# Optimization experiments

Measured on AMD Instinct MI355X. Metric: run time of the kernel, lower is better.

## Reference

```python
import jax, jax.numpy as jnp
import numpy as np

N_SRC, N_DST, E = 10000, 10000, 640000
S, T, O, H = 128, 128, 128, 4
D = O // H


def setup_inputs() -> dict:
    key = jax.random.key(0)
    ks = jax.random.split(key, 12)
    f = lambda k, shape, fan: jax.random.normal(k, shape, dtype=jnp.float32) / np.float32(np.sqrt(fan))
    return {
        "x_src": jax.random.normal(ks[0], (N_SRC, S), dtype=jnp.float32),
        "x_dst": jax.random.normal(ks[1], (N_DST, T), dtype=jnp.float32),
        "W_pred1": f(ks[2], (S, T), T),
        "b_pred1": jnp.zeros((S,), jnp.float32),
        "W_pred2": f(ks[3], (S, S), S),
        "b_pred2": jnp.zeros((S,), jnp.float32),
        "W_res": f(ks[4], (H * D, S), S),
        "W_src": f(ks[5], (H * D, S), S),
        "W_dst": f(ks[6], (H * D, T), T),
        "att_src": jax.random.normal(ks[7], (1, H, D), dtype=jnp.float32) * 0.01,
        "att_dst": jax.random.normal(ks[8], (1, H, D), dtype=jnp.float32) * 0.01,
        "W_self": f(ks[9], (H * D, T), T),
        "b_self": jnp.zeros((H * D,), jnp.float32),
        "edge_src": jax.random.randint(ks[10], (E,), 0, N_SRC),
        "edge_dst": jax.random.randint(ks[11], (E,), 0, N_DST),
        "num_dst": N_DST,
    }


def reference(x_src, x_dst, W_pred1, b_pred1, W_pred2, b_pred2, W_res, W_src, W_dst,
              att_src, att_dst, W_self, b_self, edge_src, edge_dst, num_dst):
    h, d = att_src.shape[1], att_src.shape[2]
    # residual prediction path: pred_mlp(x_dst) = Lin2(ReLU(Lin1(x_dst)))
    pred = jax.nn.relu(x_dst @ W_pred1.T + b_pred1) @ W_pred2.T + b_pred2  # [Ndst,S]
    residual = x_src[edge_src] - pred[edge_dst]                            # [E,S]
    # per-node attention logits (equivalent to gather-then-dot, cheaper)
    a_s = ((x_src @ W_src.T).reshape(-1, h, d) * att_src).sum(-1)          # [Nsrc,H]
    a_d = ((x_dst @ W_dst.T).reshape(-1, h, d) * att_dst).sum(-1)          # [Ndst,H]
    alpha = jax.nn.leaky_relu(a_s[edge_src] + a_d[edge_dst], 0.2)          # [E,H]
    # edge softmax over incoming edges of each destination node
    amax = jax.ops.segment_max(alpha, edge_dst, num_segments=num_dst)      # [Ndst,H]
    ex = jnp.exp(alpha - amax[edge_dst])
    denom = jax.ops.segment_sum(ex, edge_dst, num_segments=num_dst)
    alpha = ex / (denom[edge_dst] + 1e-16)                                 # [E,H]
    # attention-weighted aggregation of transformed residuals
    msg = (residual @ W_res.T).reshape(-1, h, d) * alpha[:, :, None]       # [E,H,D]
    agg = jax.ops.segment_sum(msg.reshape(-1, h * d), edge_dst, num_segments=num_dst)
    return agg + x_dst @ W_self.T + b_self                                 # [Ndst,H*D]
```

## Files before the change

### kernel.cpp

```cpp
#include <hip/hip_runtime.h>
#include <hip/hip_bf16.h>

#define LEAKY 0.2f
#define CAP 160
#define CAPB 8192
#define CHUNK 2048
#define GSTRIDE 32

#define FMA4(A, S, V) do { (A).x += (S)*(V).x; (A).y += (S)*(V).y; (A).z += (S)*(V).z; (A).w += (S)*(V).w; } while (0)

typedef __attribute__((ext_vector_type(8))) short bf16x8;
typedef __attribute__((ext_vector_type(4))) float f32x4;

struct GemmJob {
  const float* X; const float* W; const float* B; float* Y;
  int M; int relu; int bf16out;
  const float* vvec;
  float* aout;
};

__device__ __forceinline__ unsigned short f2bf(float f) {
  unsigned int u = __float_as_uint(f);
  u += 0x7FFFu + ((u >> 16) & 1u);
  return (unsigned short)(u >> 16);
}
__device__ __forceinline__ float bf2f(unsigned short h) {
  return __uint_as_float(((unsigned int)h) << 16);
}

__device__ __forceinline__ bf16x8 pack8(const float4& a, const float4& b) {
  bf16x8 r;
  r[0] = (short)__builtin_bit_cast(unsigned short, __float2bfloat16(a.x));
  r[1] = (short)__builtin_bit_cast(unsigned short, __float2bfloat16(a.y));
  r[2] = (short)__builtin_bit_cast(unsigned short, __float2bfloat16(a.z));
  r[3] = (short)__builtin_bit_cast(unsigned short, __float2bfloat16(a.w));
  r[4] = (short)__builtin_bit_cast(unsigned short, __float2bfloat16(b.x));
  r[5] = (short)__builtin_bit_cast(unsigned short, __float2bfloat16(b.y));
  r[6] = (short)__builtin_bit_cast(unsigned short, __float2bfloat16(b.z));
  r[7] = (short)__builtin_bit_cast(unsigned short, __float2bfloat16(b.w));
  return r;
}

__device__ __forceinline__ void gemm128_mfma(
    const float* __restrict__ X, const float* __restrict__ W,
    const float* __restrict__ B, float* __restrict__ Y,
    int M, int relu, int bf16out, int row0,
    const float* __restrict__ vvec, float* __restrict__ aout) {
  if (row0 >= M) return;
  const int tid = threadIdx.x;
  const int wv = tid >> 6;
  const int ln = tid & 63;
  const int lr = ln & 15;
  const int kg = ln >> 4;

  const f32x4 zero = {0.f, 0.f, 0.f, 0.f};
  f32x4 acc[2][8];
#pragma unroll
  for (int mt = 0; mt < 2; mt++)
#pragma unroll
    for (int nt = 0; nt < 8; nt++) acc[mt][nt] = zero;

  float4 av0 = make_float4(0.f, 0.f, 0.f, 0.f), av1 = av0;

  const int r0 = row0 + wv * 32 + lr;
  const int r1 = r0 + 16;
  const int rc0 = r0 < M ? r0 : M - 1;
  const int rc1 = r1 < M ? r1 : M - 1;
  const float* xp0 = X + (size_t)rc0 * 128 + kg * 8;
  const float* xp1 = X + (size_t)rc1 * 128 + kg * 8;
  const float* wp  = W + (size_t)lr * 128 + kg * 8;

#pragma unroll
  for (int k0 = 0; k0 < 128; k0 += 32) {
    float4 xa0 = *(const float4*)(xp0 + k0);
    float4 xb0 = *(const float4*)(xp0 + k0 + 4);
    float4 xa1 = *(const float4*)(xp1 + k0);
    float4 xb1 = *(const float4*)(xp1 + k0 + 4);
    bf16x8 a0 = pack8(xa0, xb0);
    bf16x8 a1 = pack8(xa1, xb1);
#pragma unroll
    for (int nt = 0; nt < 8; nt++) {
      const float* wq = wp + (size_t)nt * 16 * 128 + k0;
      bf16x8 bw = pack8(*(const float4*)wq, *(const float4*)(wq + 4));
      acc[0][nt] = __builtin_amdgcn_mfma_f32_16x16x32_bf16(a0, bw, acc[0][nt], 0, 0, 0);
      acc[1][nt] = __builtin_amdgcn_mfma_f32_16x16x32_bf16(a1, bw, acc[1][nt], 0, 0, 0);
    }
    if (vvec) {
      const float4* vv = (const float4*)vvec + (k0 + kg * 8);
#pragma unroll
      for (int j = 0; j < 4; j++) {
        float4 v4 = vv[j];
        float s0 = (j == 0) ? xa0.x : (j == 1) ? xa0.y : (j == 2) ? xa0.z : xa0.w;
        float s1 = (j == 0) ? xa1.x : (j == 1) ? xa1.y : (j == 2) ? xa1.z : xa1.w;
        FMA4(av0, s0, v4); FMA4(av1, s1, v4);
      }
#pragma unroll
      for (int j = 0; j < 4; j++) {
        float4 v4 = vv[4 + j];
        float s0 = (j == 0) ? xb0.x : (j == 1) ? xb0.y : (j == 2) ? xb0.z : xb0.w;
        float s1 = (j == 0) ? xb1.x : (j == 1) ? xb1.y : (j == 2) ? xb1.z : xb1.w;
        FMA4(av0, s0, v4); FMA4(av1, s1, v4);
      }
    }
  }

  if (vvec) {
    av0.x += __shfl_xor(av0.x, 16, 64); av0.y += __shfl_xor(av0.y, 16, 64);
    av0.z += __shfl_xor(av0.z, 16, 64); av0.w += __shfl_xor(av0.w, 16, 64);
    av0.x += __shfl_xor(av0.x, 32, 64); av0.y += __shfl_xor(av0.y, 32, 64);
    av0.z += __shfl_xor(av0.z, 32, 64); av0.w += __shfl_xor(av0.w, 32, 64);
    av1.x += __shfl_xor(av1.x, 16, 64); av1.y += __shfl_xor(av1.y, 16, 64);
    av1.z += __shfl_xor(av1.z, 16, 64); av1.w += __shfl_xor(av1.w, 16, 64);
    av1.x += __shfl_xor(av1.x, 32, 64); av1.y += __shfl_xor(av1.y, 32, 64);
    av1.z += __shfl_xor(av1.z, 32, 64); av1.w += __shfl_xor(av1.w, 32, 64);
    if (kg == 0) {
      if (r0 < M) *(float4*)(aout + (size_t)r0 * 4) = av0;
      if (r1 < M) *(float4*)(aout + (size_t)r1 * 4) = av1;
    }
  }

  float bv[8];
#pragma unroll
  for (int nt = 0; nt < 8; nt++) bv[nt] = B ? B[nt * 16 + lr] : 0.f;

  const int rbase = row0 + wv * 32 + kg * 4;
#pragma unroll
  for (int mt = 0; mt < 2; mt++) {
#pragma unroll
    for (int i = 0; i < 4; i++) {
      int r = rbase + mt * 16 + i;
      if (r >= M) continue;
      if (bf16out) {
        unsigned short* yb = (unsigned short*)Y + (size_t)r * 128 + lr;
#pragma unroll
        for (int nt = 0; nt < 8; nt++) {
          float o = acc[mt][nt][i] + bv[nt];
          if (relu) o = fmaxf(o, 0.f);
          yb[nt * 16] = f2bf(o);
        }
      } else {
        float* yp = Y + (size_t)r * 128 + lr;
#pragma unroll
        for (int nt = 0; nt < 8; nt++) {
          float o = acc[mt][nt][i] + bv[nt];
          if (relu) o = fmaxf(o, 0.f);
          yp[nt * 16] = o;
        }
      }
    }
  }
}

__global__ __launch_bounds__(256) void phase1(
    const float* __restrict__ Wsrc, const float* __restrict__ attsrc,
    const float* __restrict__ Wdst, const float* __restrict__ attdst,
    const float* __restrict__ W_res, const float* __restrict__ W2,
    const float* __restrict__ b2,
    GemmJob jA,
    float* __restrict__ v_src, float* __restrict__ v_dst,
    float* __restrict__ Wc, float* __restrict__ bc,
    const int* __restrict__ edge_src, const int* __restrict__ edge_dst,
    int* __restrict__ gcnt, int* __restrict__ bin,
    int E, int Nd, int NB, int GA, int Q1, int T1) {
  __shared__ int bsm[CHUNK + 3 * CAP];
  int bx = blockIdx.x, tid = threadIdx.x;
  int u = (bx & 7) * Q1 + (bx >> 3);
  if (u >= T1) return;
  if (u == 0) {
    int which = tid >> 7, k = tid & 127;
    const float* W = which ? Wdst : Wsrc;
    const float* att = which ? attdst : attsrc;
    float* v = which ? v_dst : v_src;
    float s[4] = {0.f, 0.f, 0.f, 0.f};
#pragma unroll
    for (int h = 0; h < 4; h++)
      for (int d = 0; d < 32; d++)
        s[h] += W[(size_t)(h * 32 + d) * 128 + k] * att[h * 32 + d];
#pragma unroll
    for (int h = 0; h < 4; h++) v[k * 4 + h] = s[h];
  } else if (u == 1) {
    if (tid < 128) {
      float s = 0.f;
      for (int i = 0; i < 128; i++) s += W_res[(size_t)tid * 128 + i] * b2[i];
      bc[tid] = s;
    }
  } else if (u < 66) {
    int id = (u - 2) * 256 + tid;
    int o = id >> 7, j = id & 127;
    float s = 0.f;
    for (int i = 0; i < 128; i++) s += W_res[(size_t)o * 128 + i] * W2[(size_t)i * 128 + j];
    Wc[(size_t)o * 128 + j] = s;
  } else if (u < 66 + GA) {
    gemm128_mfma(jA.X, jA.W, jA.B, jA.Y, jA.M, jA.relu, jA.bf16out,
                 (u - 66) * 128, jA.vvec, jA.aout);
  } else {
    int* pk    = bsm;
    int* hist  = bsm + CHUNK;
    int* gbase = hist + CAP;
    int* lcur  = gbase + CAP;
    int e0 = (u - 66 - GA) * CHUNK;
    int n = E - e0; if (n > CHUNK) n = CHUNK;
    if (n <= 0) return;
    for (int i = tid; i < NB; i += 256) hist[i] = 0;
    __syncthreads();
    for (int i = tid; i < n; i += 256) {
      int s = edge_src[e0 + i], d = edge_dst[e0 + i];
      pk[i] = (s << 14) | d;
      atomicAdd(&hist[d >> 6], 1);
    }
    __syncthreads();
    for (int b = tid; b < NB; b += 256) {
      gbase[b] = hist[b] ? atomicAdd(&gcnt[b * GSTRIDE], hist[b]) : 0;
      lcur[b] = 0;
    }
    __syncthreads();
    for (int i = tid; i < n; i += 256) {
      int p = pk[i];
      int b = (p & 16383) >> 6;
      int off = gbase[b] + atomicAdd(&lcur[b], 1);
      if (off < CAPB) bin[(size_t)b * CAPB + off] = p;
    }
  }
}

__global__ __launch_bounds__(256) void phase2(
    GemmJob j0, GemmJob j1, GemmJob j2,
    const int* __restrict__ gcnt, const int* __restrict__ bin,
    int* __restrict__ sorted_src, int* __restrict__ rstart, int* __restrict__ rend,
    int Nd, int G, int Q2, int T2) {
  __shared__ int ssm[128];
  int bx = blockIdx.x, tid = threadIdx.x;
  int u = (bx % 6) * Q2 + bx / 6;
  if (u >= T2) return;
  if (u < 3 * G) {
    GemmJob J = (u < G) ? j0 : (u < 2 * G) ? j1 : j2;
    gemm128_mfma(J.X, J.W, J.B, J.Y, J.M, J.relu, J.bf16out, (u % G) * 128, J.vvec, J.aout);
  } else {
    int b = u - 3 * G;
    int* hist2 = ssm;
    int* lcur2 = ssm + 64;
    int cnt = gcnt[b * GSTRIDE]; if (cnt > CAPB) cnt = CAPB;
    size_t base = (size_t)b * CAPB;
    if (tid < 64) hist2[tid] = 0;
    __syncthreads();
    for (int i = tid; i < cnt; i += 256) atomicAdd(&hist2[bin[base + i] & 63], 1);
    __syncthreads();
    if (tid < 64) {
      int v = hist2[tid];
      int incl = v;
#pragma unroll
      for (int off = 1; off < 64; off <<= 1) {
        int t = __shfl_up(incl, off, 64);
        if (tid >= off) incl += t;
      }
      int st = incl - v;
      lcur2[tid] = st;
      int dst = (b << 6) + tid;
      if (dst < Nd) {
        rstart[dst] = (int)base + st;
        rend[dst]   = (int)base + st + v;
      }
    }
    __syncthreads();
    for (int i = tid; i < cnt; i += 256) {
      int p = bin[base + i];
      int j = p & 63;
      int lp = atomicAdd(&lcur2[j], 1);
      sorted_src[base + lp] = p >> 14;
    }
  }
}

__global__ __launch_bounds__(256) void phase3(
    const int* __restrict__ rstart, const int* __restrict__ rend,
    const int* __restrict__ sorted_src,
    const float* __restrict__ a_s, const float* __restrict__ a_d,
    const unsigned short* __restrict__ u_src, const float* __restrict__ u_pred,
    const float* __restrict__ self_o, float* __restrict__ out, int Nd) {
  __shared__ float smem[1920];
  int bx = blockIdx.x, tid = threadIdx.x;
  int half = tid >> 7;
  int t = tid & 127;
  int dst = bx * 2 + half;
  if (dst >= Nd) return;

  float* wbuf  = smem + half * 640;
  int* srcbuf  = (int*)(smem + 1280) + half * 160;
  float4* red4 = (float4*)(smem + 1600);
  float4* redv = (float4*)(smem + 1616) + half * 32;
  float* inv_s = smem + 1872 + half * 4;
  float* sA_s  = smem + 1880 + half * 4;

  int start = rstart[dst];
  int deg = rend[dst] - start;
  float4 ad4 = *(const float4*)(a_d + (size_t)dst * 4);
  float s0 = 0.f, s1 = 0.f, s2 = 0.f, s3 = 0.f;
  for (int i = t; i < deg; i += 128) {
    int src = sorted_src[start + i];
    float4 as4 = *(const float4*)(a_s + (size_t)src * 4);
    float l0 = as4.x + ad4.x; l0 = l0 > 0.f ? l0 : LEAKY * l0;
    float l1 = as4.y + ad4.y; l1 = l1 > 0.f ? l1 : LEAKY * l1;
    float l2 = as4.z + ad4.z; l2 = l2 > 0.f ? l2 : LEAKY * l2;
    float l3 = as4.w + ad4.w; l3 = l3 > 0.f ? l3 : LEAKY * l3;
    float w0 = __expf(l0), w1 = __expf(l1), w2 = __expf(l2), w3 = __expf(l3);
    if (i < CAP) {
      wbuf[i * 4 + 0] = w0; wbuf[i * 4 + 1] = w1;
      wbuf[i * 4 + 2] = w2; wbuf[i * 4 + 3] = w3;
      srcbuf[i] = src;
    }
    s0 += w0; s1 += w1; s2 += w2; s3 += w3;
  }
  int wave = tid >> 6;
#pragma unroll
  for (int off = 32; off > 0; off >>= 1) {
    s0 += __shfl_xor(s0, off, 64);
    s1 += __shfl_xor(s1, off, 64);
    s2 += __shfl_xor(s2, off, 64);
    s3 += __shfl_xor(s3, off, 64);
  }
  if ((tid & 63) == 0) red4[wave] = make_float4(s0, s1, s2, s3);
  __syncthreads();
  if (t == 0) {
    float4 A = red4[half * 2], B = red4[half * 2 + 1];
    float dx = A.x + B.x, dy = A.y + B.y, dz = A.z + B.z, dw = A.w + B.w;
    inv_s[0] = 1.f / (dx + 1e-16f); sA_s[0] = dx * inv_s[0];
    inv_s[1] = 1.f / (dy + 1e-16f); sA_s[1] = dy * inv_s[1];
    inv_s[2] = 1.f / (dz + 1e-16f); sA_s[2] = dz * inv_s[2];
    inv_s[3] = 1.f / (dw + 1e-16f); sA_s[3] = dw * inv_s[3];
  }
  __syncthreads();

  int c4 = t & 31, rgrp = t >> 5, h = c4 >> 3;
  int coff = c4 * 4;
  float4 acc0 = make_float4(0.f,0.f,0.f,0.f), acc1 = acc0, acc2 = acc0, acc3 = acc0;
  int cap = deg < CAP ? deg : CAP;
  int i = rgrp;
  for (; i + 12 < cap; i += 16) {
    int sA = srcbuf[i], sB = srcbuf[i + 4], sC = srcbuf[i + 8], sD = srcbuf[i + 12];
    float wA = wbuf[i * 4 + h], wB = wbuf[(i + 4) * 4 + h];
    float wC = wbuf[(i + 8) * 4 + h], wD = wbuf[(i + 12) * 4 + h];
    ushort4 hA = *(const ushort4*)(u_src + (size_t)sA * 128 + coff);
    ushort4 hB = *(const ushort4*)(u_src + (size_t)sB * 128 + coff);
    ushort4 hC = *(const ushort4*)(u_src + (size_t)sC * 128 + coff);
    ushort4 hD = *(const ushort4*)(u_src + (size_t)sD * 128 + coff);
    float4 uA = make_float4(bf2f(hA.x), bf2f(hA.y), bf2f(hA.z), bf2f(hA.w));
    float4 uB = make_float4(bf2f(hB.x), bf2f(hB.y), bf2f(hB.z), bf2f(hB.w));
    float4 uC = make_float4(bf2f(hC.x), bf2f(hC.y), bf2f(hC.z), bf2f(hC.w));
    float4 uD = make_float4(bf2f(hD.x), bf2f(hD.y), bf2f(hD.z), bf2f(hD.w));
    FMA4(acc0, wA, uA); FMA4(acc1, wB, uB); FMA4(acc2, wC, uC); FMA4(acc3, wD, uD);
  }
  for (; i < cap; i += 4) {
    int s_ = srcbuf[i];
    float w = wbuf[i * 4 + h];
    ushort4 hh = *(const ushort4*)(u_src + (size_t)s_ * 128 + coff);
    float4 uu = make_float4(bf2f(hh.x), bf2f(hh.y), bf2f(hh.z), bf2f(hh.w));
    FMA4(acc0, w, uu);
  }
  if (deg > CAP) {
    float adh = (h == 0) ? ad4.x : (h == 1) ? ad4.y : (h == 2) ? ad4.z : ad4.w;
    for (int k = CAP + rgrp; k < deg; k += 4) {
      int src = sorted_src[start + k];
      float l = a_s[(size_t)src * 4 + h] + adh;
      l = l > 0.f ? l : LEAKY * l;
      float w = __expf(l);
      ushort4 hh = *(const ushort4*)(u_src + (size_t)src * 128 + coff);
      float4 uu = make_float4(bf2f(hh.x), bf2f(hh.y), bf2f(hh.z), bf2f(hh.w));
      FMA4(acc0, w, uu);
    }
  }
  float4 acc;
  acc.x = acc0.x + acc1.x + acc2.x + acc3.x;
  acc.y = acc0.y + acc1.y + acc2.y + acc3.y;
  acc.z = acc0.z + acc1.z + acc2.z + acc3.z;
  acc.w = acc0.w + acc1.w + acc2.w + acc3.w;
  acc.x += __shfl_xor(acc.x, 32, 64);
  acc.y += __shfl_xor(acc.y, 32, 64);
  acc.z += __shfl_xor(acc.z, 32, 64);
  acc.w += __shfl_xor(acc.w, 32, 64);
  if (t >= 64 && t < 96) redv[c4] = acc;
  __syncthreads();
  if (t < 32) {
    float4 r = redv[c4];
    acc.x += r.x; acc.y += r.y; acc.z += r.z; acc.w += r.w;
    float4 up = *(const float4*)(u_pred + (size_t)dst * 128 + coff);
    float4 so = *(const float4*)(self_o + (size_t)dst * 128 + coff);
    float iv = inv_s[h], sa = sA_s[h];
    float4 o;
    o.x = acc.x * iv - sa * up.x + so.x;
    o.y = acc.y * iv - sa * up.y + so.y;
    o.z = acc.z * iv - sa * up.z + so.z;
    o.w = acc.w * iv - sa * up.w + so.w;
    *(float4*)(out + (size_t)dst * 128 + coff) = o;
  }
}

extern "C" void kernel_launch(void* const* d_in, const int* in_sizes, int n_in,
                              void* d_out, int out_size, void* d_ws, size_t ws_size,
                              hipStream_t stream) {
  const float* x_src   = (const float*)d_in[0];
  const float* x_dst   = (const float*)d_in[1];
  const float* W_pred1 = (const float*)d_in[2];
  const float* b_pred1 = (const float*)d_in[3];
  const float* W_pred2 = (const float*)d_in[4];
  const float* b_pred2 = (const float*)d_in[5];
  const float* W_res   = (const float*)d_in[6];
  const float* W_src   = (const float*)d_in[7];
  const float* W_dst   = (const float*)d_in[8];
  const float* att_src = (const float*)d_in[9];
  const float* att_dst = (const float*)d_in[10];
  const float* W_self  = (const float*)d_in[11];
  const float* b_self  = (const float*)d_in[12];
  const int* edge_src  = (const int*)d_in[13];
  const int* edge_dst  = (const int*)d_in[14];
  int Ns = in_sizes[0] / 128;
  int Nd = in_sizes[1] / 128;
  int E  = in_sizes[13];
  float* out = (float*)d_out;
  int NB = (Nd + 63) >> 6;

  char* ws = (char*)d_ws;
  auto alloc = [&](size_t bytes) -> char* {
    char* p = ws;
    ws += (bytes + 255) & ~(size_t)255;
    return p;
  };
  float* relu1  = (float*)alloc((size_t)Nd * 128 * 4);
  unsigned short* u_src = (unsigned short*)alloc((size_t)Ns * 128 * 2);
  float* u_pred = (float*)alloc((size_t)Nd * 128 * 4);
  float* self_o = (float*)alloc((size_t)Nd * 128 * 4);
  float* a_s    = (float*)alloc((size_t)Ns * 4 * 4);
  float* a_d    = (float*)alloc((size_t)Nd * 4 * 4);
  float* v_src  = (float*)alloc(128 * 4 * 4);
  float* v_dst  = (float*)alloc(128 * 4 * 4);
  float* Wc     = (float*)alloc(128 * 128 * 4);
  float* bc     = (float*)alloc(128 * 4);
  int* gcnt     = (int*)alloc((size_t)NB * GSTRIDE * 4);
  int* rstart   = (int*)alloc((size_t)Nd * 4);
  int* rend     = (int*)alloc((size_t)Nd * 4);
  int* bin      = (int*)alloc((size_t)NB * CAPB * 4);
  int* sorted_src = (int*)alloc((size_t)NB * CAPB * 4);

  hipMemsetAsync(gcnt, 0, (size_t)NB * GSTRIDE * sizeof(int), stream);

  int GA  = (Nd + 127) / 128;
  int NCH = (E + CHUNK - 1) / CHUNK;
  int T1 = 66 + GA + NCH;
  int Q1 = (T1 + 7) / 8;
  GemmJob jA{ x_dst, W_pred1, b_pred1, relu1, Nd, 1, 0, nullptr, nullptr };
  hipLaunchKernelGGL(phase1, dim3(Q1 * 8), dim3(256), 0, stream,
                     W_src, att_src, W_dst, att_dst, W_res, W_pred2, b_pred2, jA,
                     v_src, v_dst, Wc, bc, edge_src, edge_dst, gcnt, bin,
                     E, Nd, NB, GA, Q1, T1);

  int maxM = Ns > Nd ? Ns : Nd;
  int G  = (maxM + 127) / 128;
  int T2 = 3 * G + NB;
  int Q2 = (T2 + 5) / 6;
  GemmJob jB{ x_src, W_res,  nullptr, (float*)u_src, Ns, 0, 1, v_src, a_s };
  GemmJob jC{ x_dst, W_self, b_self,  self_o, Nd, 0, 0, v_dst, a_d };
  GemmJob jU{ relu1, Wc,     bc,      u_pred, Nd, 0, 0, nullptr, nullptr };
  hipLaunchKernelGGL(phase2, dim3(Q2 * 6), dim3(256), 0, stream,
                     jB, jC, jU, gcnt, bin, sorted_src, rstart, rend,
                     Nd, G, Q2, T2);

  hipLaunchKernelGGL(phase3, dim3((Nd + 1) / 2), dim3(256), 0, stream,
                     rstart, rend, sorted_src, a_s, a_d, u_src, u_pred, self_o, out, Nd);
}
```

Baseline: 157.3 us.

## Fuse three phases into one persistent cooperative kernel with grid syncs

Replaces the three separate kernel launches with one persistent cooperative kernel of up to 512 blocks. Each block loops over work units and the three stages are separated by grid.sync, with a fallback to three launches of a staged kernel. It also recomputes the attention projection vectors inside each GEMM unit rather than in a separate unit, moves the x_src/x_dst GEMMs into the first stage, and doubles the edge-binning chunk size. The aim is to remove launch gaps and tail idle time between phases. The costs are grid-barrier overhead, a fixed grid-stride loop that may balance work worse, redundant per-tile projection work, and possible occupancy limits from launch_bounds(256,2).

New measurement: 383.9 us. +144.1%, slower.

```diff
diff --git a/kernel.cpp b/kernel.cpp
--- a/kernel.cpp
+++ b/kernel.cpp
@@ -1,11 +1,15 @@
 #include <hip/hip_runtime.h>
 #include <hip/hip_bf16.h>
+#include <hip/hip_cooperative_groups.h>
+
+namespace cg = cooperative_groups;
 
 #define LEAKY 0.2f
 #define CAP 160
 #define CAPB 8192
-#define CHUNK 2048
+#define CHUNK 4096
 #define GSTRIDE 32
+#define GRID 512
 
 #define FMA4(A, S, V) do { (A).x += (S)*(V).x; (A).y += (S)*(V).y; (A).z += (S)*(V).z; (A).w += (S)*(V).w; } while (0)
 
@@ -15,8 +19,21 @@
 struct GemmJob {
   const float* X; const float* W; const float* B; float* Y;
   int M; int relu; int bf16out;
-  const float* vvec;
+  const float* Wv;
+  const float* attv;
   float* aout;
+};
+
+struct Params {
+  GemmJob jA, jB, jC, jU;
+  const float* W_res; const float* W2; const float* b2;
+  float* Wc; float* bc;
+  const int* edge_src; const int* edge_dst;
+  int* gcnt; int* bin; int* sorted_src; int* rstart; int* rend;
+  const float* a_s; const float* a_d;
+  const unsigned short* u_src; const float* u_pred; const float* self_o;
+  float* out;
+  int E, Nd, NB, GA, G, NCH, U0, U1, U2;
 };
 
 __device__ __forceinline__ unsigned short f2bf(float f) {
@@ -45,7 +62,7 @@
     const float* __restrict__ X, const float* __restrict__ W,
     const float* __restrict__ B, float* __restrict__ Y,
     int M, int relu, int bf16out, int row0,
-    const float* __restrict__ vvec, float* __restrict__ aout) {
+    const float* vvec, float* __restrict__ aout) {
   if (row0 >= M) return;
   const int tid = threadIdx.x;
   const int wv = tid >> 6;
@@ -151,138 +168,97 @@
   }
 }
 
-__global__ __launch_bounds__(256) void phase1(
-    const float* __restrict__ Wsrc, const float* __restrict__ attsrc,
-    const float* __restrict__ Wdst, const float* __restrict__ attdst,
-    const float* __restrict__ W_res, const float* __restrict__ W2,
-    const float* __restrict__ b2,
-    GemmJob jA,
-    float* __restrict__ v_src, float* __restrict__ v_dst,
-    float* __restrict__ Wc, float* __restrict__ bc,
-    const int* __restrict__ edge_src, const int* __restrict__ edge_dst,
-    int* __restrict__ gcnt, int* __restrict__ bin,
-    int E, int Nd, int NB, int GA, int Q1, int T1) {
-  __shared__ int bsm[CHUNK + 3 * CAP];
-  int bx = blockIdx.x, tid = threadIdx.x;
-  int u = (bx & 7) * Q1 + (bx >> 3);
-  if (u >= T1) return;
-  if (u == 0) {
-    int which = tid >> 7, k = tid & 127;
-    const float* W = which ? Wdst : Wsrc;
-    const float* att = which ? attdst : attsrc;
-    float* v = which ? v_dst : v_src;
-    float s[4] = {0.f, 0.f, 0.f, 0.f};
-#pragma unroll
-    for (int h = 0; h < 4; h++)
-      for (int d = 0; d < 32; d++)
-        s[h] += W[(size_t)(h * 32 + d) * 128 + k] * att[h * 32 + d];
-#pragma unroll
-    for (int h = 0; h < 4; h++) v[k * 4 + h] = s[h];
-  } else if (u == 1) {
-    if (tid < 128) {
+__device__ __forceinline__ void gemm_unit(const GemmJob& J, int row0, char* smemraw) {
+  const float* vvec = nullptr;
+  if (J.Wv) {
+    float* vl = (float*)smemraw;
+    for (int idx = threadIdx.x; idx < 512; idx += 256) {
+      int k = idx >> 2, h = idx & 3;
+      const float* wp = J.Wv + (size_t)(h * 32) * 128 + k;
+      const float* ap = J.attv + h * 32;
       float s = 0.f;
-      for (int i = 0; i < 128; i++) s += W_res[(size_t)tid * 128 + i] * b2[i];
-      bc[tid] = s;
-    }
-  } else if (u < 66) {
-    int id = (u - 2) * 256 + tid;
-    int o = id >> 7, j = id & 127;
-    float s = 0.f;
-    for (int i = 0; i < 128; i++) s += W_res[(size_t)o * 128 + i] * W2[(size_t)i * 128 + j];
-    Wc[(size_t)o * 128 + j] = s;
-  } else if (u < 66 + GA) {
-    gemm128_mfma(jA.X, jA.W, jA.B, jA.Y, jA.M, jA.relu, jA.bf16out,
-                 (u - 66) * 128, jA.vvec, jA.aout);
-  } else {
-    int* pk    = bsm;
-    int* hist  = bsm + CHUNK;
-    int* gbase = hist + CAP;
-    int* lcur  = gbase + CAP;
-    int e0 = (u - 66 - GA) * CHUNK;
-    int n = E - e0; if (n > CHUNK) n = CHUNK;
-    if (n <= 0) return;
-    for (int i = tid; i < NB; i += 256) hist[i] = 0;
+#pragma unroll 8
+      for (int d = 0; d < 32; d++) s += wp[(size_t)d * 128] * ap[d];
+      vl[idx] = s;
+    }
     __syncthreads();
-    for (int i = tid; i < n; i += 256) {
-      int s = edge_src[e0 + i], d = edge_dst[e0 + i];
-      pk[i] = (s << 14) | d;
-      atomicAdd(&hist[d >> 6], 1);
-    }
-    __syncthreads();
-    for (int b = tid; b < NB; b += 256) {
-      gbase[b] = hist[b] ? atomicAdd(&gcnt[b * GSTRIDE], hist[b]) : 0;
-      lcur[b] = 0;
-    }
-    __syncthreads();
-    for (int i = tid; i < n; i += 256) {
-      int p = pk[i];
-      int b = (p & 16383) >> 6;
-      int off = gbase[b] + atomicAdd(&lcur[b], 1);
-      if (off < CAPB) bin[(size_t)b * CAPB + off] = p;
-    }
-  }
-}
-
-__global__ __launch_bounds__(256) void phase2(
-    GemmJob j0, GemmJob j1, GemmJob j2,
-    const int* __restrict__ gcnt, const int* __restrict__ bin,
-    int* __restrict__ sorted_src, int* __restrict__ rstart, int* __restrict__ rend,
-    int Nd, int G, int Q2, int T2) {
-  __shared__ int ssm[128];
-  int bx = blockIdx.x, tid = threadIdx.x;
-  int u = (bx % 6) * Q2 + bx / 6;
-  if (u >= T2) return;
-  if (u < 3 * G) {
-    GemmJob J = (u < G) ? j0 : (u < 2 * G) ? j1 : j2;
-    gemm128_mfma(J.X, J.W, J.B, J.Y, J.M, J.relu, J.bf16out, (u % G) * 128, J.vvec, J.aout);
-  } else {
-    int b = u - 3 * G;
-    int* hist2 = ssm;
-    int* lcur2 = ssm + 64;
-    int cnt = gcnt[b * GSTRIDE]; if (cnt > CAPB) cnt = CAPB;
-    size_t base = (size_t)b * CAPB;
-    if (tid < 64) hist2[tid] = 0;
-    __syncthreads();
-    for (int i = tid; i < cnt; i += 256) atomicAdd(&hist2[bin[base + i] & 63], 1);
-    __syncthreads();
-    if (tid < 64) {
-      int v = hist2[tid];
-      int incl = v;
-#pragma unroll
-      for (int off = 1; off < 64; off <<= 1) {
-        int t = __shfl_up(incl, off, 64);
-        if (tid >= off) incl += t;
-      }
-      int st = incl - v;
-      lcur2[tid] = st;
-      int dst = (b << 6) + tid;
-      if (dst < Nd) {
-        rstart[dst] = (int)base + st;
-        rend[dst]   = (int)base + st + v;
-      }
-    }
-    __syncthreads();
-    for (int i = tid; i < cnt; i += 256) {
-      int p = bin[base + i];
-      int j = p & 63;
-      int lp = atomicAdd(&lcur2[j], 1);
-      sorted_src[base + lp] = p >> 14;
-    }
-  }
-}
-
-__global__ __launch_bounds__(256) void phase3(
-    const int* __restrict__ rstart, const int* __restrict__ rend,
-    const int* __restrict__ sorted_src,
-    const float* __restrict__ a_s, const float* __restrict__ a_d,
-    const unsigned short* __restrict__ u_src, const float* __restrict__ u_pred,
-    const float* __restrict__ self_o, float* __restrict__ out, int Nd) {
-  __shared__ float smem[1920];
-  int bx = blockIdx.x, tid = threadIdx.x;
+    vvec = vl;
+  }
+  gemm128_mfma(J.X, J.W, J.B, J.Y, J.M, J.relu, J.bf16out, row0, vvec, J.aout);
+}
+
+__device__ __forceinline__ void bin_unit(const Params& P, int c, char* smemraw) {
+  int* pk    = (int*)smemraw;
+  int* hist  = pk + CHUNK;
+  int* gbase = hist + CAP;
+  int* lcur  = gbase + CAP;
+  const int tid = threadIdx.x;
+  int e0 = c * CHUNK;
+  int n = P.E - e0; if (n > CHUNK) n = CHUNK;
+  for (int i = tid; i < P.NB; i += 256) hist[i] = 0;
+  __syncthreads();
+  for (int i = tid; i < n; i += 256) {
+    int s = P.edge_src[e0 + i], d = P.edge_dst[e0 + i];
+    pk[i] = (s << 14) | d;
+    atomicAdd(&hist[d >> 6], 1);
+  }
+  __syncthreads();
+  for (int b = tid; b < P.NB; b += 256) {
+    gbase[b] = hist[b] ? atomicAdd(&P.gcnt[b * GSTRIDE], hist[b]) : 0;
+    lcur[b] = 0;
+  }
+  __syncthreads();
+  for (int i = tid; i < n; i += 256) {
+    int p = pk[i];
+    int b = (p & 16383) >> 6;
+    int off = gbase[b] + atomicAdd(&lcur[b], 1);
+    if (off < CAPB) P.bin[(size_t)b * CAPB + off] = p;
+  }
+}
+
+__device__ __forceinline__ void sort_unit(const Params& P, int b, char* smemraw) {
+  int* hist2 = (int*)smemraw;
+  int* lcur2 = hist2 + 64;
+  const int tid = threadIdx.x;
+  int cnt = P.gcnt[b * GSTRIDE]; if (cnt > CAPB) cnt = CAPB;
+  size_t base = (size_t)b * CAPB;
+  if (tid < 64) hist2[tid] = 0;
+  __syncthreads();
+  for (int i = tid; i < cnt; i += 256) atomicAdd(&hist2[P.bin[base + i] & 63], 1);
+  __syncthreads();
+  if (tid < 64) {
+    int v = hist2[tid];
+    int incl = v;
+#pragma unroll
+    for (int off = 1; off < 64; off <<= 1) {
+      int t = __shfl_up(incl, off, 64);
+      if (tid >= off) incl += t;
+    }
+    int st = incl - v;
+    lcur2[tid] = st;
+    int dst = (b << 6) + tid;
+    if (dst < P.Nd) {
+      P.rstart[dst] = (int)base + st;
+      P.rend[dst]   = (int)base + st + v;
+    }
+  }
+  __syncthreads();
+  for (int i = tid; i < cnt; i += 256) {
+    int p = P.bin[base + i];
+    int j = p & 63;
+    int lp = atomicAdd(&lcur2[j], 1);
+    P.sorted_src[base + lp] = p >> 14;
+  }
+}
+
+__device__ __forceinline__ void agg_unit(const Params& P, int unit, char* smemraw) {
+  float* smem = (float*)smemraw;
+  const int tid = threadIdx.x;
   int half = tid >> 7;
   int t = tid & 127;
-  int dst = bx * 2 + half;
-  if (dst >= Nd) return;
+  int dst = unit * 2 + half;
+  bool act = dst < P.Nd;
+  int dstc = act ? dst : P.Nd - 1;
 
   float* wbuf  = smem + half * 640;
   int* srcbuf  = (int*)(smem + 1280) + half * 160;
@@ -291,13 +267,13 @@
   float* inv_s = smem + 1872 + half * 4;
   float* sA_s  = smem + 1880 + half * 4;
 
-  int start = rstart[dst];
-  int deg = rend[dst] - start;
-  float4 ad4 = *(const float4*)(a_d + (size_t)dst * 4);
+  int start = P.rstart[dstc];
+  int deg = act ? (P.rend[dstc] - start) : 0;
+  float4 ad4 = *(const float4*)(P.a_d + (size_t)dstc * 4);
   float s0 = 0.f, s1 = 0.f, s2 = 0.f, s3 = 0.f;
   for (int i = t; i < deg; i += 128) {
-    int src = sorted_src[start + i];
-    float4 as4 = *(const float4*)(a_s + (size_t)src * 4);
+    int src = P.sorted_src[start + i];
+    float4 as4 = *(const float4*)(P.a_s + (size_t)src * 4);
     float l0 = as4.x + ad4.x; l0 = l0 > 0.f ? l0 : LEAKY * l0;
     float l1 = as4.y + ad4.y; l1 = l1 > 0.f ? l1 : LEAKY * l1;
     float l2 = as4.z + ad4.z; l2 = l2 > 0.f ? l2 : LEAKY * l2;
@@ -339,10 +315,10 @@
     int sA = srcbuf[i], sB = srcbuf[i + 4], sC = srcbuf[i + 8], sD = srcbuf[i + 12];
     float wA = wbuf[i * 4 + h], wB = wbuf[(i + 4) * 4 + h];
     float wC = wbuf[(i + 8) * 4 + h], wD = wbuf[(i + 12) * 4 + h];
-    ushort4 hA = *(const ushort4*)(u_src + (size_t)sA * 128 + coff);
-    ushort4 hB = *(const ushort4*)(u_src + (size_t)sB * 128 + coff);
-    ushort4 hC = *(const ushort4*)(u_src + (size_t)sC * 128 + coff);
-    ushort4 hD = *(const ushort4*)(u_src + (size_t)sD * 128 + coff);
+    ushort4 hA = *(const ushort4*)(P.u_src + (size_t)sA * 128 + coff);
+    ushort4 hB = *(const ushort4*)(P.u_src + (size_t)sB * 128 + coff);
+    ushort4 hC = *(const ushort4*)(P.u_src + (size_t)sC * 128 + coff);
+    ushort4 hD = *(const ushort4*)(P.u_src + (size_t)sD * 128 + coff);
     float4 uA = make_float4(bf2f(hA.x), bf2f(hA.y), bf2f(hA.z), bf2f(hA.w));
     float4 uB = make_float4(bf2f(hB.x), bf2f(hB.y), bf2f(hB.z), bf2f(hB.w));
     float4 uC = make_float4(bf2f(hC.x), bf2f(hC.y), bf2f(hC.z), bf2f(hC.w));
@@ -352,18 +328,18 @@
   for (; i < cap; i += 4) {
     int s_ = srcbuf[i];
     float w = wbuf[i * 4 + h];
-    ushort4 hh = *(const ushort4*)(u_src + (size_t)s_ * 128 + coff);
+    ushort4 hh = *(const ushort4*)(P.u_src + (size_t)s_ * 128 + coff);
     float4 uu = make_float4(bf2f(hh.x), bf2f(hh.y), bf2f(hh.z), bf2f(hh.w));
     FMA4(acc0, w, uu);
   }
   if (deg > CAP) {
     float adh = (h == 0) ? ad4.x : (h == 1) ? ad4.y : (h == 2) ? ad4.z : ad4.w;
     for (int k = CAP + rgrp; k < deg; k += 4) {
-      int src = sorted_src[start + k];
-      float l = a_s[(size_t)src * 4 + h] + adh;
+      int src = P.sorted_src[start + k];
+      float l = P.a_s[(size_t)src * 4 + h] + adh;
       l = l > 0.f ? l : LEAKY * l;
       float w = __expf(l);
-      ushort4 hh = *(const ushort4*)(u_src + (size_t)src * 128 + coff);
+      ushort4 hh = *(const ushort4*)(P.u_src + (size_t)src * 128 + coff);
       float4 uu = make_float4(bf2f(hh.x), bf2f(hh.y), bf2f(hh.z), bf2f(hh.w));
       FMA4(acc0, w, uu);
     }
@@ -379,19 +355,78 @@
   acc.w += __shfl_xor(acc.w, 32, 64);
   if (t >= 64 && t < 96) redv[c4] = acc;
   __syncthreads();
-  if (t < 32) {
+  if (t < 32 && act) {
     float4 r = redv[c4];
     acc.x += r.x; acc.y += r.y; acc.z += r.z; acc.w += r.w;
-    float4 up = *(const float4*)(u_pred + (size_t)dst * 128 + coff);
-    float4 so = *(const float4*)(self_o + (size_t)dst * 128 + coff);
+    float4 up = *(const float4*)(P.u_pred + (size_t)dst * 128 + coff);
+    float4 so = *(const float4*)(P.self_o + (size_t)dst * 128 + coff);
     float iv = inv_s[h], sa = sA_s[h];
     float4 o;
     o.x = acc.x * iv - sa * up.x + so.x;
     o.y = acc.y * iv - sa * up.y + so.y;
     o.z = acc.z * iv - sa * up.z + so.z;
     o.w = acc.w * iv - sa * up.w + so.w;
-    *(float4*)(out + (size_t)dst * 128 + coff) = o;
-  }
+    *(float4*)(P.out + (size_t)dst * 128 + coff) = o;
+  }
+}
+
+__device__ __forceinline__ void run_stage(const Params& P, int stage, char* smemraw,
+                                          int bid, int grd) {
+  const int tid = threadIdx.x;
+  if (stage == 0) {
+    for (int u = bid; u < P.U0; u += grd) {
+      __syncthreads();
+      if (u < 64) {
+        int id = u * 256 + tid;
+        int o = id >> 7, j = id & 127;
+        float s = 0.f;
+        for (int i = 0; i < 128; i++) s += P.W_res[(size_t)o * 128 + i] * P.W2[(size_t)i * 128 + j];
+        P.Wc[(size_t)o * 128 + j] = s;
+      } else if (u == 64) {
+        if (tid < 128) {
+          float s = 0.f;
+          for (int i = 0; i < 128; i++) s += P.W_res[(size_t)tid * 128 + i] * P.b2[i];
+          P.bc[tid] = s;
+        }
+      } else if (u < 65 + P.GA) {
+        gemm_unit(P.jA, (u - 65) * 128, smemraw);
+      } else if (u < 65 + P.GA + P.G) {
+        gemm_unit(P.jB, (u - 65 - P.GA) * 128, smemraw);
+      } else if (u < 65 + P.GA + 2 * P.G) {
+        gemm_unit(P.jC, (u - 65 - P.GA - P.G) * 128, smemraw);
+      } else {
+        bin_unit(P, u - (65 + P.GA + 2 * P.G), smemraw);
+      }
+    }
+  } else if (stage == 1) {
+    for (int u = bid; u < P.U1; u += grd) {
+      __syncthreads();
+      if (u < P.G) gemm_unit(P.jU, u * 128, smemraw);
+      else sort_unit(P, u - P.G, smemraw);
+    }
+  } else {
+    for (int u = bid; u < P.U2; u += grd) {
+      __syncthreads();
+      agg_unit(P, u, smemraw);
+    }
+  }
+}
+
+__global__ __launch_bounds__(256, 2) void kmain(Params P) {
+  __shared__ __align__(16) char smemraw[18816];
+  cg::grid_group grid = cg::this_grid();
+  run_stage(P, 0, smemraw, blockIdx.x, gridDim.x);
+  __threadfence();
+  grid.sync();
+  run_stage(P, 1, smemraw, blockIdx.x, gridDim.x);
+  __threadfence();
+  grid.sync();
+  run_stage(P, 2, smemraw, blockIdx.x, gridDim.x);
+}
+
+__global__ __launch_bounds__(256, 2) void kstage(Params P, int stage) {
+  __shared__ __align__(16) char smemraw[18816];
+  run_stage(P, stage, smemraw, blockIdx.x, gridDim.x);
 }
 
 extern "C" void kernel_launch(void* const* d_in, const int* in_sizes, int n_in,
@@ -430,8 +465,6 @@
   float* self_o = (float*)alloc((size_t)Nd * 128 * 4);
   float* a_s    = (float*)alloc((size_t)Ns * 4 * 4);
   float* a_d    = (float*)alloc((size_t)Nd * 4 * 4);
-  float* v_src  = (float*)alloc(128 * 4 * 4);
-  float* v_dst  = (float*)alloc(128 * 4 * 4);
   float* Wc     = (float*)alloc(128 * 128 * 4);
   float* bc     = (float*)alloc(128 * 4);
   int* gcnt     = (int*)alloc((size_t)NB * GSTRIDE * 4);
@@ -443,26 +476,53 @@
   hipMemsetAsync(gcnt, 0, (size_t)NB * GSTRIDE * sizeof(int), stream);
 
   int GA  = (Nd + 127) / 128;
+  int maxM = Ns > Nd ? Ns : Nd;
+  int G   = (maxM + 127) / 128;
   int NCH = (E + CHUNK - 1) / CHUNK;
-  int T1 = 66 + GA + NCH;
-  int Q1 = (T1 + 7) / 8;
-  GemmJob jA{ x_dst, W_pred1, b_pred1, relu1, Nd, 1, 0, nullptr, nullptr };
-  hipLaunchKernelGGL(phase1, dim3(Q1 * 8), dim3(256), 0, stream,
-                     W_src, att_src, W_dst, att_dst, W_res, W_pred2, b_pred2, jA,
-                     v_src, v_dst, Wc, bc, edge_src, edge_dst, gcnt, bin,
-                     E, Nd, NB, GA, Q1, T1);
-
-  int maxM = Ns > Nd ? Ns : Nd;
-  int G  = (maxM + 127) / 128;
-  int T2 = 3 * G + NB;
-  int Q2 = (T2 + 5) / 6;
-  GemmJob jB{ x_src, W_res,  nullptr, (float*)u_src, Ns, 0, 1, v_src, a_s };
-  GemmJob jC{ x_dst, W_self, b_self,  self_o, Nd, 0, 0, v_dst, a_d };
-  GemmJob jU{ relu1, Wc,     bc,      u_pred, Nd, 0, 0, nullptr, nullptr };
-  hipLaunchKernelGGL(phase2, dim3(Q2 * 6), dim3(256), 0, stream,
-                     jB, jC, jU, gcnt, bin, sorted_src, rstart, rend,
-                     Nd, G, Q2, T2);
-
-  hipLaunchKernelGGL(phase3, dim3((Nd + 1) / 2), dim3(256), 0, stream,
-                     rstart, rend, sorted_src, a_s, a_d, u_src, u_pred, self_o, out, Nd);
-}
+
+  Params P;
+  P.jA = GemmJob{ x_dst, W_pred1, b_pred1, relu1, Nd, 1, 0, nullptr, nullptr, nullptr };
+  P.jB = GemmJob{ x_src, W_res,  nullptr, (float*)u_src, Ns, 0, 1, W_src, att_src, a_s };
+  P.jC = GemmJob{ x_dst, W_self, b_self,  self_o, Nd, 0, 0, W_dst, att_dst, a_d };
+  P.jU = GemmJob{ relu1, Wc,     bc,      u_pred, Nd, 0, 0, nullptr, nullptr, nullptr };
+  P.W_res = W_res; P.W2 = W_pred2; P.b2 = b_pred2;
+  P.Wc = Wc; P.bc = bc;
+  P.edge_src = edge_src; P.edge_dst = edge_dst;
+  P.gcnt = gcnt; P.bin = bin; P.sorted_src = sorted_src;
+  P.rstart = rstart; P.rend = rend;
+  P.a_s = a_s; P.a_d = a_d;
+  P.u_src = u_src; P.u_pred = u_pred; P.self_o = self_o;
+  P.out = out;
+  P.E = E; P.Nd = Nd; P.NB = NB; P.GA = GA; P.G = G; P.NCH = NCH;
+  P.U0 = 65 + GA + 2 * G + NCH;
+  P.U1 = G + NB;
+  P.U2 = (Nd + 1) / 2;
+
+  static int coopGrid = -2;
+  if (coopGrid == -2) {
+    int occ = 0, numCU = 256;
+    hipDeviceProp_t prop;
+    if (hipGetDeviceProperties(&prop, 0) == hipSuccess && prop.multiProcessorCount > 0)
+      numCU = prop.multiProcessorCount;
+    if (hipOccupancyMaxActiveBlocksPerMultiprocessor(&occ, kmain, 256, 0) == hipSuccess && occ > 0) {
+      long cap = (long)occ * numCU;
+      coopGrid = cap > GRID ? GRID : (int)cap;
+    } else {
+      coopGrid = -1;
+    }
+  }
+
+  bool done = false;
+  if (coopGrid > 0) {
+    void* args[] = { (void*)&P };
+    hipError_t le = hipLaunchCooperativeKernel((const void*)kmain, dim3(coopGrid), dim3(256),
+                                               args, 0, stream);
+    if (le == hipSuccess) done = true;
+    else coopGrid = -1;
+  }
+  if (!done) {
+    hipLaunchKernelGGL(kstage, dim3(GRID), dim3(256), 0, stream, P, 0);
+    hipLaunchKernelGGL(kstage, dim3(GRID), dim3(256), 0, stream, P, 1);
+    hipLaunchKernelGGL(kstage, dim3(GRID), dim3(256), 0, stream, P, 2);
+  }
+}
```

## Stage counting-sort scatters in shared memory for coalesced global writes

Applied to the files above, without the earlier changes.

The binning in phase1 and the per-bin sort in phase2 now scatter elements into a shared-memory staging buffer using local prefix offsets, then write them to global memory in order. Before, each element went straight to a random global position. This is meant to turn those scattered stores into contiguous, coalesced writes. The cost is much more LDS: phase2 now holds about 33KB per block (8192 ints), which may reduce occupancy for the GEMM blocks that share that kernel, and phase1 passes nullptr for the vvec/aout arguments of its GEMM call.

New measurement: 158.7 us, median of 2. No clear change (+0.9%).

```diff
diff --git a/kernel.cpp b/kernel.cpp
--- a/kernel.cpp
+++ b/kernel.cpp
@@ -45,7 +45,7 @@
     const float* __restrict__ X, const float* __restrict__ W,
     const float* __restrict__ B, float* __restrict__ Y,
     int M, int relu, int bf16out, int row0,
-    const float* __restrict__ vvec, float* __restrict__ aout) {
+    const float* vvec, float* __restrict__ aout) {
   if (row0 >= M) return;
   const int tid = threadIdx.x;
   const int wv = tid >> 6;
@@ -162,7 +162,7 @@
     const int* __restrict__ edge_src, const int* __restrict__ edge_dst,
     int* __restrict__ gcnt, int* __restrict__ bin,
     int E, int Nd, int NB, int GA, int Q1, int T1) {
-  __shared__ int bsm[CHUNK + 3 * CAP];
+  __shared__ __align__(16) int bsm[2 * CHUNK + 4 * CAP];
   int bx = blockIdx.x, tid = threadIdx.x;
   int u = (bx & 7) * Q1 + (bx >> 3);
   if (u >= T1) return;
@@ -192,12 +192,14 @@
     Wc[(size_t)o * 128 + j] = s;
   } else if (u < 66 + GA) {
     gemm128_mfma(jA.X, jA.W, jA.B, jA.Y, jA.M, jA.relu, jA.bf16out,
-                 (u - 66) * 128, jA.vvec, jA.aout);
+                 (u - 66) * 128, nullptr, nullptr);
   } else {
-    int* pk    = bsm;
-    int* hist  = bsm + CHUNK;
-    int* gbase = hist + CAP;
-    int* lcur  = gbase + CAP;
+    int* pk      = bsm;
+    int* lsorted = pk + CHUNK;
+    int* hist    = lsorted + CHUNK;
+    int* gbase   = hist + CAP;
+    int* lstart  = gbase + CAP;
+    int* lcur    = lstart + CAP;
     int e0 = (u - 66 - GA) * CHUNK;
     int n = E - e0; if (n > CHUNK) n = CHUNK;
     if (n <= 0) return;
@@ -209,15 +211,35 @@
       atomicAdd(&hist[d >> 6], 1);
     }
     __syncthreads();
-    for (int b = tid; b < NB; b += 256) {
+    for (int b = tid; b < NB; b += 256)
       gbase[b] = hist[b] ? atomicAdd(&gcnt[b * GSTRIDE], hist[b]) : 0;
-      lcur[b] = 0;
+    if (tid < 64) {
+      int PB = (NB + 63) >> 6;
+      int sl = 0;
+      for (int k = 0; k < PB; k++) { int idx = tid * PB + k; if (idx < NB) sl += hist[idx]; }
+      int incl = sl;
+#pragma unroll
+      for (int off = 1; off < 64; off <<= 1) {
+        int tv = __shfl_up(incl, off, 64);
+        if (tid >= off) incl += tv;
+      }
+      int run = incl - sl;
+      for (int k = 0; k < PB; k++) {
+        int idx = tid * PB + k;
+        if (idx < NB) { lstart[idx] = run; lcur[idx] = run; run += hist[idx]; }
+      }
     }
     __syncthreads();
     for (int i = tid; i < n; i += 256) {
       int p = pk[i];
       int b = (p & 16383) >> 6;
-      int off = gbase[b] + atomicAdd(&lcur[b], 1);
+      lsorted[atomicAdd(&lcur[b], 1)] = p;
+    }
+    __syncthreads();
+    for (int j = tid; j < n; j += 256) {
+      int p = lsorted[j];
+      int b = (p & 16383) >> 6;
+      int off = gbase[b] + (j - lstart[b]);
       if (off < CAPB) bin[(size_t)b * CAPB + off] = p;
     }
   }
@@ -228,7 +250,7 @@
     const int* __restrict__ gcnt, const int* __restrict__ bin,
     int* __restrict__ sorted_src, int* __restrict__ rstart, int* __restrict__ rend,
     int Nd, int G, int Q2, int T2) {
-  __shared__ int ssm[128];
+  __shared__ __align__(16) int ssm[CAPB + 192];
   int bx = blockIdx.x, tid = threadIdx.x;
   int u = (bx % 6) * Q2 + bx / 6;
   if (u >= T2) return;
@@ -237,8 +259,10 @@
     gemm128_mfma(J.X, J.W, J.B, J.Y, J.M, J.relu, J.bf16out, (u % G) * 128, J.vvec, J.aout);
   } else {
     int b = u - 3 * G;
-    int* hist2 = ssm;
-    int* lcur2 = ssm + 64;
+    int* lsorted = ssm;
+    int* hist2   = lsorted + CAPB;
+    int* lstart2 = hist2 + 64;
+    int* lcur2   = lstart2 + 64;
     int cnt = gcnt[b * GSTRIDE]; if (cnt > CAPB) cnt = CAPB;
     size_t base = (size_t)b * CAPB;
     if (tid < 64) hist2[tid] = 0;
@@ -250,11 +274,11 @@
       int incl = v;
 #pragma unroll
       for (int off = 1; off < 64; off <<= 1) {
-        int t = __shfl_up(incl, off, 64);
-        if (tid >= off) incl += t;
+        int tv = __shfl_up(incl, off, 64);
+        if (tid >= off) incl += tv;
       }
       int st = incl - v;
-      lcur2[tid] = st;
+      lstart2[tid] = st; lcur2[tid] = st;
       int dst = (b << 6) + tid;
       if (dst < Nd) {
         rstart[dst] = (int)base + st;
@@ -264,10 +288,11 @@
     __syncthreads();
     for (int i = tid; i < cnt; i += 256) {
       int p = bin[base + i];
-      int j = p & 63;
-      int lp = atomicAdd(&lcur2[j], 1);
-      sorted_src[base + lp] = p >> 14;
-    }
+      lsorted[atomicAdd(&lcur2[p & 63], 1)] = p >> 14;
+    }
+    __syncthreads();
+    for (int i = tid; i < cnt; i += 256)
+      sorted_src[base + i] = lsorted[i];
   }
 }
 
```
